# Kernel optimization log

Hardware: AMD Instinct MI355X
Metric: run time of the kernel (lower is better)

## Reference

```python
import jax, jax.numpy as jnp
import numpy as np

V, E, H = 50000, 200, 256
B, R, S, W = 16, 16, 16, 32


def gru_last(x, Wih, Whh, bih, bhh):
    """PyTorch-style GRU, return final hidden state.
    x: [N, T, D]; Wih: [3H, D]; Whh: [3H, H]. Gate order: r, z, n."""
    gx = jnp.einsum('ntd,gd->ntg', x, Wih) + bih  # precompute input gates [N,T,3H]
    h0 = jnp.zeros((x.shape[0], Whh.shape[1]), x.dtype)

    def step(h, gxt):
        gh = h @ Whh.T + bhh
        xr, xz, xn = jnp.split(gxt, 3, axis=-1)
        hr, hz, hn = jnp.split(gh, 3, axis=-1)
        r = jax.nn.sigmoid(xr + hr)
        z = jax.nn.sigmoid(xz + hz)
        n = jnp.tanh(xn + r * hn)
        return (1.0 - z) * n + z * h, None

    h, _ = jax.lax.scan(step, h0, jnp.swapaxes(gx, 0, 1))
    return h  # [N, H]


def mlp(x, W1, b1, W2, b2):
    # Linear -> SELU -> (Dropout is identity in eval) -> Linear
    return jax.nn.selu(x @ W1.T + b1) @ W2.T + b2


def setup_inputs() -> dict:
    key = jax.random.key(0)
    ks = jax.random.split(key, 20)
    n = lambda k, shp: (jax.random.normal(k, shp, dtype=jnp.float32) * 0.05)
    inp = {
        'inputs': jax.random.randint(ks[0], (B, R, S, W), 0, V, dtype=jnp.int64),
        'emb': n(ks[1], (V, E)),
        'w_Wih': n(ks[2], (3 * H, E)), 'w_Whh': n(ks[3], (3 * H, H)),
        'w_bih': n(ks[4], (3 * H,)), 'w_bhh': n(ks[5], (3 * H,)),
        's_Wih': n(ks[6], (3 * H, H)), 's_Whh': n(ks[7], (3 * H, H)),
        's_bih': n(ks[8], (3 * H,)), 's_bhh': n(ks[9], (3 * H,)),
        'r_Wih': n(ks[10], (3 * H, H)), 'r_Whh': n(ks[11], (3 * H, H)),
        'r_bih': n(ks[12], (3 * H,)), 'r_bhh': n(ks[13], (3 * H,)),
        'rfc_W1': n(ks[14], (H // 2, H)), 'rfc_b1': n(ks[15], (H // 2,)),
        'rfc_W2': n(ks[16], (1, H // 2)), 'rfc_b2': jnp.zeros((1,), jnp.float32),
        'pfc_W1': n(ks[17], (H // 2, H)), 'pfc_b1': n(ks[18], (H // 2,)),
        'pfc_W2': n(ks[19], (1, H // 2)), 'pfc_b2': jnp.zeros((1,), jnp.float32),
    }
    return inp


def reference(inputs, emb, w_Wih, w_Whh, w_bih, w_bhh,
              s_Wih, s_Whh, s_bih, s_bhh,
              r_Wih, r_Whh, r_bih, r_bhh,
              rfc_W1, rfc_b1, rfc_W2, rfc_b2,
              pfc_W1, pfc_b1, pfc_W2, pfc_b2):
    b, r, s, w = inputs.shape
    x = emb[inputs]                                   # [B,R,S,W,E] (dropout = identity in eval)
    # word-level GRU over all sentences at once (batches the Python double loop)
    sent_h = gru_last(x.reshape(b * r * s, w, E), w_Wih, w_Whh, w_bih, w_bhh)  # [B*R*S, H]
    # sentence-level GRU per review
    rev_h = gru_last(sent_h.reshape(b * r, s, H), s_Wih, s_Whh, s_bih, s_bhh)  # [B*R, H]
    p_batch = rev_h.reshape(b, r, H)                  # [B, R, H]
    r_stars = mlp(p_batch, rfc_W1, rfc_b1, rfc_W2, rfc_b2)  # [B, R, 1]
    # review-level GRU per business
    biz_h = gru_last(p_batch, r_Wih, r_Whh, r_bih, r_bhh)   # [B, H]
    b_stars = mlp(biz_h, pfc_W1, pfc_b1, pfc_W2, pfc_b2)    # [B, 1]
    return (b_stars, r_stars)
```

## Files before the change

### kernel.cpp

```cpp
#include <hip/hip_runtime.h>
#include <math.h>

#define VOCAB 50000
#define EDIM  200
#define HDIM  256
#define G3    768
#define NSEQ1 4096
#define T1    32
#define NSEQ2 256
#define T2    16
#define NSEQ3 16
#define T3    16

using bf16x8 = __attribute__((ext_vector_type(8))) short;
using f32x4  = __attribute__((ext_vector_type(4))) float;

__device__ __forceinline__ float sigmoid_f(float x) {
    return 1.0f / (1.0f + __expf(-x));
}
__device__ __forceinline__ float tanh_f(float x) {
    return 1.0f - 2.0f / (__expf(2.0f * x) + 1.0f);
}
__device__ __forceinline__ short f2b(float f) {
    unsigned u = __float_as_uint(f);
    unsigned r = (u + 0x7fffu + ((u >> 16) & 1u)) >> 16;
    return (short)r;
}

__global__ void convert_pad(const float* __restrict__ src, short* __restrict__ dst,
                            int Kin, int Kpad) {
    const int r = blockIdx.x;
    for (int k = threadIdx.x; k < Kpad; k += blockDim.x)
        dst[(size_t)r * Kpad + k] = (k < Kin) ? f2b(src[(size_t)r * Kin + k]) : (short)0;
}

template <int KC, bool AF32>
__global__ __launch_bounds__(512) void gemm_mfma(
    const void* __restrict__ Av, const short* __restrict__ WB,
    const float* __restrict__ bias, float* __restrict__ C,
    int M, int Keff) {
    constexpr int KPAD  = KC * 32;
    constexpr int CELLS = KPAD / 8;
    __shared__ short As[128 * 256];
    const int tid = threadIdx.x;
    const int m0 = blockIdx.x * 128;
    const int n0 = blockIdx.y * 192;

    {
        const int row  = tid >> 2;
        const int c0   = (tid & 3) * 8;
        const int rowg = m0 + row;
        const int vcell = Keff >> 3;
        for (int i = 0; i < 8; i++) {
            const int c = c0 + i;
            if (c >= CELLS) break;
            bf16x8 v;
            if (rowg < M && c < vcell) {
                if constexpr (AF32) {
                    const float* ap = (const float*)Av + (size_t)rowg * Keff + c * 8;
                    const float4 x = *(const float4*)ap;
                    const float4 y = *(const float4*)(ap + 4);
                    v[0] = f2b(x.x); v[1] = f2b(x.y); v[2] = f2b(x.z); v[3] = f2b(x.w);
                    v[4] = f2b(y.x); v[5] = f2b(y.y); v[6] = f2b(y.z); v[7] = f2b(y.w);
                } else {
                    const short* ap = (const short*)Av + (size_t)rowg * Keff + c * 8;
                    v = *(const bf16x8*)ap;
                }
            } else {
                v = (bf16x8)(short)0;
            }
            *(bf16x8*)&As[row * 256 + ((c ^ (row & 7)) << 3)] = v;
        }
    }
    __syncthreads();

    const int w  = tid >> 6;
    const int l  = tid & 63;
    const int lr = l & 15, lg = l >> 4;

    bf16x8 af[KC];
    {
        const int row = (w << 4) + lr;
#pragma unroll
        for (int kc = 0; kc < KC; kc++) {
            const int cell = kc * 4 + lg;
            af[kc] = *(const bf16x8*)&As[row * 256 + ((cell ^ (row & 7)) << 3)];
        }
    }
    f32x4 acc[12];
#pragma unroll
    for (int nt = 0; nt < 12; nt++) acc[nt] = (f32x4){0.f, 0.f, 0.f, 0.f};
#pragma unroll
    for (int nt = 0; nt < 12; nt++) {
        const short* wb = WB + (size_t)(n0 + nt * 16 + lr) * KPAD + lg * 8;
#pragma unroll
        for (int kc = 0; kc < KC; kc++) {
            bf16x8 bf = *(const bf16x8*)(wb + kc * 32);
            acc[nt] = __builtin_amdgcn_mfma_f32_16x16x32_bf16(af[kc], bf, acc[nt], 0, 0, 0);
        }
    }
#pragma unroll
    for (int nt = 0; nt < 12; nt++) {
        const int col = n0 + nt * 16 + lr;
        const float bv = bias[col];
#pragma unroll
        for (int q = 0; q < 4; q++) {
            const int row = m0 + (w << 4) + lg * 4 + q;
            if (row < M) C[(size_t)row * G3 + col] = acc[nt][q] + bv;
        }
    }
}

__global__ __launch_bounds__(512) void gru_mfma(
    const int* __restrict__ idx,
    const float* __restrict__ gxsrc,
    const short* __restrict__ WB,
    const float* __restrict__ bhh,
    float* __restrict__ hf32,
    short* __restrict__ hb16,
    int T) {
    __shared__ short hsB[16 * 256];
    const int tid = threadIdx.x;
    const int n0 = blockIdx.x * 16;
    const int w  = tid >> 6, l = tid & 63;
    const int lr = l & 15, lg = l >> 4;
    const int tt0 = w * 2;

    for (int i = tid; i < 16 * 256; i += 512) hsB[i] = 0;

    float bR[2], bZ[2], bN[2];
#pragma unroll
    for (int ti = 0; ti < 2; ti++) {
        const int jj = (tt0 + ti) * 16 + lr;
        bR[ti] = bhh[jj]; bZ[ti] = bhh[256 + jj]; bN[ti] = bhh[512 + jj];
    }
    float hreg[2][4] = {};
    int toks[4];
    if (idx) {
#pragma unroll
        for (int q = 0; q < 4; q++) toks[q] = idx[(size_t)(n0 + lg * 4 + q) * T];
    }
    __syncthreads();

    for (int t = 0; t < T; t++) {
        float gxv[2][4][3];
#pragma unroll
        for (int q = 0; q < 4; q++) {
            const size_t rowbase = idx ? (size_t)toks[q] * G3
                                       : ((size_t)(n0 + lg * 4 + q) * T + t) * G3;
#pragma unroll
            for (int ti = 0; ti < 2; ti++) {
                const int jj = (tt0 + ti) * 16 + lr;
                gxv[ti][q][0] = gxsrc[rowbase + jj];
                gxv[ti][q][1] = gxsrc[rowbase + 256 + jj];
                gxv[ti][q][2] = gxsrc[rowbase + 512 + jj];
            }
        }
        bf16x8 af[8];
#pragma unroll
        for (int kc = 0; kc < 8; kc++) {
            const int cell = kc * 4 + lg;
            af[kc] = *(const bf16x8*)&hsB[lr * 256 + ((cell ^ (lr & 7)) << 3)];
        }
        __syncthreads();

        f32x4 acc[2][3];
#pragma unroll
        for (int ti = 0; ti < 2; ti++)
#pragma unroll
            for (int g = 0; g < 3; g++) acc[ti][g] = (f32x4){0.f, 0.f, 0.f, 0.f};
#pragma unroll
        for (int ti = 0; ti < 2; ti++) {
#pragma unroll
            for (int g = 0; g < 3; g++) {
                const short* wb = WB + (size_t)(g * 256 + (tt0 + ti) * 16 + lr) * 256 + lg * 8;
#pragma unroll
                for (int kc = 0; kc < 8; kc++) {
                    bf16x8 bf = *(const bf16x8*)(wb + kc * 32);
                    acc[ti][g] = __builtin_amdgcn_mfma_f32_16x16x32_bf16(af[kc], bf, acc[ti][g], 0, 0, 0);
                }
            }
        }
        if (idx && t + 1 < T) {
#pragma unroll
            for (int q = 0; q < 4; q++) toks[q] = idx[(size_t)(n0 + lg * 4 + q) * T + t + 1];
        }
#pragma unroll
        for (int ti = 0; ti < 2; ti++) {
            const int jj = (tt0 + ti) * 16 + lr;
#pragma unroll
            for (int q = 0; q < 4; q++) {
                const float r = sigmoid_f(gxv[ti][q][0] + acc[ti][0][q] + bR[ti]);
                const float z = sigmoid_f(gxv[ti][q][1] + acc[ti][1][q] + bZ[ti]);
                const float n = tanh_f(gxv[ti][q][2] + r * (acc[ti][2][q] + bN[ti]));
                const float h = (1.f - z) * n + z * hreg[ti][q];
                hreg[ti][q] = h;
                const int s = lg * 4 + q;
                hsB[s * 256 + (((jj >> 3) ^ (s & 7)) << 3) + (jj & 7)] = f2b(h);
            }
        }
        __syncthreads();
    }
#pragma unroll
    for (int ti = 0; ti < 2; ti++) {
        const int jj = (tt0 + ti) * 16 + lr;
#pragma unroll
        for (int q = 0; q < 4; q++) {
            const int s = lg * 4 + q;
            const size_t o = (size_t)(n0 + s) * HDIM + jj;
            if (hf32) hf32[o] = hreg[ti][q];
            if (hb16) hb16[o] = f2b(hreg[ti][q]);
        }
    }
}

__global__ __launch_bounds__(128) void mlp_head(
    const float* __restrict__ hin, const float* __restrict__ W1,
    const float* __restrict__ b1, const float* __restrict__ W2,
    const float* __restrict__ b2, float* __restrict__ out) {
    const int row = blockIdx.x;
    const int gg = threadIdx.x;
    const float* h = hin + (size_t)row * HDIM;
    const float* wv1 = W1 + (size_t)gg * HDIM;
    float acc = 0.f;
#pragma unroll 4
    for (int k = 0; k < HDIM; k += 4) {
        const float4 hv = *(const float4*)&h[k];
        const float4 wv = *(const float4*)&wv1[k];
        acc += hv.x * wv.x; acc += hv.y * wv.y;
        acc += hv.z * wv.z; acc += hv.w * wv.w;
    }
    acc += b1[gg];
    const float alpha = 1.6732632423543772f;
    const float scale = 1.0507009873554805f;
    const float s = scale * (acc > 0.f ? acc : alpha * expm1f(acc));
    float v = s * W2[gg];

    __shared__ float red[128];
    red[gg] = v;
    __syncthreads();
    if (gg < 64) {
        float x = red[gg] + red[gg + 64];
#pragma unroll
        for (int off = 32; off; off >>= 1) x += __shfl_down(x, off);
        if (gg == 0) out[row] = x + b2[0];
    }
}

extern "C" void kernel_launch(void* const* d_in, const int* in_sizes, int n_in,
                              void* d_out, int out_size, void* d_ws, size_t ws_size,
                              hipStream_t stream) {
    const int*   idx    = (const int*)d_in[0];
    const float* emb    = (const float*)d_in[1];
    const float* w_Wih  = (const float*)d_in[2];
    const float* w_Whh  = (const float*)d_in[3];
    const float* w_bih  = (const float*)d_in[4];
    const float* w_bhh  = (const float*)d_in[5];
    const float* s_Wih  = (const float*)d_in[6];
    const float* s_Whh  = (const float*)d_in[7];
    const float* s_bih  = (const float*)d_in[8];
    const float* s_bhh  = (const float*)d_in[9];
    const float* r_Wih  = (const float*)d_in[10];
    const float* r_Whh  = (const float*)d_in[11];
    const float* r_bih  = (const float*)d_in[12];
    const float* r_bhh  = (const float*)d_in[13];
    const float* rfc_W1 = (const float*)d_in[14];
    const float* rfc_b1 = (const float*)d_in[15];
    const float* rfc_W2 = (const float*)d_in[16];
    const float* rfc_b2 = (const float*)d_in[17];
    const float* pfc_W1 = (const float*)d_in[18];
    const float* pfc_b1 = (const float*)d_in[19];
    const float* pfc_W2 = (const float*)d_in[20];
    const float* pfc_b2 = (const float*)d_in[21];

    float* out = (float*)d_out;

    float* fws = (float*)d_ws;
    float* P     = fws;
    float* gx2   = P     + (size_t)VOCAB * G3;
    float* rev_h = gx2   + (size_t)NSEQ1 * G3;
    float* gx3   = rev_h + (size_t)NSEQ2 * HDIM;
    float* biz_h = gx3   + (size_t)NSEQ2 * G3;
    short* sws = (short*)(biz_h + (size_t)NSEQ3 * HDIM);
    short* WhhB_w = sws;
    short* WihB_w = WhhB_w + (size_t)G3 * HDIM;
    short* sWihB  = WihB_w + (size_t)G3 * 224;
    short* sWhhB  = sWihB  + (size_t)G3 * HDIM;
    short* rWihB  = sWhhB  + (size_t)G3 * HDIM;
    short* rWhhB  = rWihB  + (size_t)G3 * HDIM;
    short* sent_hB = rWhhB + (size_t)G3 * HDIM;
    short* rev_hB  = sent_hB + (size_t)NSEQ1 * HDIM;

    convert_pad<<<G3, 256, 0, stream>>>(w_Whh, WhhB_w, HDIM, HDIM);
    convert_pad<<<G3, 256, 0, stream>>>(w_Wih, WihB_w, EDIM, 224);
    convert_pad<<<G3, 256, 0, stream>>>(s_Wih, sWihB, HDIM, HDIM);
    convert_pad<<<G3, 256, 0, stream>>>(s_Whh, sWhhB, HDIM, HDIM);
    convert_pad<<<G3, 256, 0, stream>>>(r_Wih, rWihB, HDIM, HDIM);
    convert_pad<<<G3, 256, 0, stream>>>(r_Whh, rWhhB, HDIM, HDIM);

    gemm_mfma<7, true><<<dim3((VOCAB + 127) / 128, 4), 512, 0, stream>>>(
        emb, WihB_w, w_bih, P, VOCAB, EDIM);

    gru_mfma<<<NSEQ1 / 16, 512, 0, stream>>>(
        idx, P, WhhB_w, w_bhh, nullptr, sent_hB, T1);

    gemm_mfma<8, false><<<dim3(NSEQ1 / 128, 4), 512, 0, stream>>>(
        sent_hB, sWihB, s_bih, gx2, NSEQ1, HDIM);

    gru_mfma<<<NSEQ2 / 16, 512, 0, stream>>>(
        nullptr, gx2, sWhhB, s_bhh, rev_h, rev_hB, T2);

    mlp_head<<<NSEQ2, 128, 0, stream>>>(
        rev_h, rfc_W1, rfc_b1, rfc_W2, rfc_b2, out + 16);

    gemm_mfma<8, false><<<dim3(2, 4), 512, 0, stream>>>(
        rev_hB, rWihB, r_bih, gx3, NSEQ2, HDIM);

    gru_mfma<<<1, 512, 0, stream>>>(
        nullptr, gx3, rWhhB, r_bhh, biz_h, nullptr, T3);

    mlp_head<<<NSEQ3, 128, 0, stream>>>(
        biz_h, pfc_W1, pfc_b1, pfc_W2, pfc_b2, out);
}
```

Baseline: 706.1 us.

## Store input-gate projections in bf16 and double-buffer them into LDS via async loads

```diff
diff --git a/kernel.cpp b/kernel.cpp
--- a/kernel.cpp
+++ b/kernel.cpp
@@ -26,6 +26,14 @@
     unsigned r = (u + 0x7fffu + ((u >> 16) & 1u)) >> 16;
     return (short)r;
 }
+__device__ __forceinline__ float b2f(unsigned short v) {
+    return __uint_as_float((unsigned)v << 16);
+}
+__device__ __forceinline__ void gload_lds16(const void* g, void* l) {
+    __builtin_amdgcn_global_load_lds(
+        (const __attribute__((address_space(1))) void*)g,
+        (__attribute__((address_space(3))) void*)l, 16, 0, 0);
+}
 
 __global__ void convert_pad(const float* __restrict__ src, short* __restrict__ dst,
                             int Kin, int Kpad) {
@@ -34,10 +42,10 @@
         dst[(size_t)r * Kpad + k] = (k < Kin) ? f2b(src[(size_t)r * Kin + k]) : (short)0;
 }
 
-template <int KC, bool AF32>
+template <int KC, bool AF32, bool CBF16>
 __global__ __launch_bounds__(512) void gemm_mfma(
     const void* __restrict__ Av, const short* __restrict__ WB,
-    const float* __restrict__ bias, float* __restrict__ C,
+    const float* __restrict__ bias, void* __restrict__ Cv,
     int M, int Keff) {
     constexpr int KPAD  = KC * 32;
     constexpr int CELLS = KPAD / 8;
@@ -106,20 +114,25 @@
 #pragma unroll
         for (int q = 0; q < 4; q++) {
             const int row = m0 + (w << 4) + lg * 4 + q;
-            if (row < M) C[(size_t)row * G3 + col] = acc[nt][q] + bv;
+            if (row < M) {
+                const float o = acc[nt][q] + bv;
+                if constexpr (CBF16) ((short*)Cv)[(size_t)row * G3 + col] = f2b(o);
+                else                 ((float*)Cv)[(size_t)row * G3 + col] = o;
+            }
         }
     }
 }
 
 __global__ __launch_bounds__(512) void gru_mfma(
     const int* __restrict__ idx,
-    const float* __restrict__ gxsrc,
+    const short* __restrict__ gxb,
     const short* __restrict__ WB,
     const float* __restrict__ bhh,
     float* __restrict__ hf32,
     short* __restrict__ hb16,
     int T) {
     __shared__ short hsB[16 * 256];
+    __shared__ short gxs[2][16 * 768];
     const int tid = threadIdx.x;
     const int n0 = blockIdx.x * 16;
     const int w  = tid >> 6, l = tid & 63;
@@ -135,34 +148,47 @@
         bR[ti] = bhh[jj]; bZ[ti] = bhh[256 + jj]; bN[ti] = bhh[512 + jj];
     }
     float hreg[2][4] = {};
-    int toks[4];
-    if (idx) {
-#pragma unroll
-        for (int q = 0; q < 4; q++) toks[q] = idx[(size_t)(n0 + lg * 4 + q) * T];
-    }
+
+    auto stage = [&](short* dstbase, int t) {
+#pragma unroll
+        for (int it = 0; it < 3; it++) {
+            const int g = it * 8192 + (tid << 4);
+            const int s = g / 1536;
+            const int cb = g - s * 1536;
+            size_t rowbase;
+            if (idx) {
+                int tk = idx[(size_t)(n0 + s) * T + t];
+                tk = min(max(tk, 0), VOCAB - 1);
+                rowbase = (size_t)tk * 1536;
+            } else {
+                rowbase = ((size_t)(n0 + s) * T + t) * 1536;
+            }
+            const int cell = cb >> 4;
+            const int sb = ((cell ^ (s & 7)) << 4) | (cb & 15);
+            const char* src = (const char*)gxb + rowbase + sb;
+            char* dst = (char*)dstbase + it * 8192 + (w << 10);
+            gload_lds16(src, dst);
+        }
+    };
+    auto gx_at = [&](const short* buf, int s, int col) -> float {
+        const int cb = col << 1;
+        const int addr = s * 1536 + ((((cb >> 4) ^ (s & 7)) << 4) | (cb & 15));
+        return b2f(*(const unsigned short*)((const char*)buf + addr));
+    };
+
+    stage(gxs[0], 0);
     __syncthreads();
 
+    int cur = 0;
     for (int t = 0; t < T; t++) {
-        float gxv[2][4][3];
-#pragma unroll
-        for (int q = 0; q < 4; q++) {
-            const size_t rowbase = idx ? (size_t)toks[q] * G3
-                                       : ((size_t)(n0 + lg * 4 + q) * T + t) * G3;
-#pragma unroll
-            for (int ti = 0; ti < 2; ti++) {
-                const int jj = (tt0 + ti) * 16 + lr;
-                gxv[ti][q][0] = gxsrc[rowbase + jj];
-                gxv[ti][q][1] = gxsrc[rowbase + 256 + jj];
-                gxv[ti][q][2] = gxsrc[rowbase + 512 + jj];
-            }
-        }
+        if (t + 1 < T) stage(gxs[cur ^ 1], t + 1);
+
         bf16x8 af[8];
 #pragma unroll
         for (int kc = 0; kc < 8; kc++) {
             const int cell = kc * 4 + lg;
             af[kc] = *(const bf16x8*)&hsB[lr * 256 + ((cell ^ (lr & 7)) << 3)];
         }
-        __syncthreads();
 
         f32x4 acc[2][3];
 #pragma unroll
@@ -181,26 +207,29 @@
                 }
             }
         }
-        if (idx && t + 1 < T) {
-#pragma unroll
-            for (int q = 0; q < 4; q++) toks[q] = idx[(size_t)(n0 + lg * 4 + q) * T + t + 1];
-        }
+        __syncthreads();
+
 #pragma unroll
         for (int ti = 0; ti < 2; ti++) {
             const int jj = (tt0 + ti) * 16 + lr;
 #pragma unroll
             for (int q = 0; q < 4; q++) {
-                const float r = sigmoid_f(gxv[ti][q][0] + acc[ti][0][q] + bR[ti]);
-                const float z = sigmoid_f(gxv[ti][q][1] + acc[ti][1][q] + bZ[ti]);
-                const float n = tanh_f(gxv[ti][q][2] + r * (acc[ti][2][q] + bN[ti]));
+                const int s = lg * 4 + q;
+                const float xr = gx_at(gxs[cur], s, jj);
+                const float xz = gx_at(gxs[cur], s, 256 + jj);
+                const float xn = gx_at(gxs[cur], s, 512 + jj);
+                const float r = sigmoid_f(xr + acc[ti][0][q] + bR[ti]);
+                const float z = sigmoid_f(xz + acc[ti][1][q] + bZ[ti]);
+                const float n = tanh_f(xn + r * (acc[ti][2][q] + bN[ti]));
                 const float h = (1.f - z) * n + z * hreg[ti][q];
                 hreg[ti][q] = h;
-                const int s = lg * 4 + q;
                 hsB[s * 256 + (((jj >> 3) ^ (s & 7)) << 3) + (jj & 7)] = f2b(h);
             }
         }
         __syncthreads();
-    }
+        cur ^= 1;
+    }
+
 #pragma unroll
     for (int ti = 0; ti < 2; ti++) {
         const int jj = (tt0 + ti) * 16 + lr;
@@ -275,21 +304,21 @@
 
     float* out = (float*)d_out;
 
-    float* fws = (float*)d_ws;
-    float* P     = fws;
-    float* gx2   = P     + (size_t)VOCAB * G3;
-    float* rev_h = gx2   + (size_t)NSEQ1 * G3;
-    float* gx3   = rev_h + (size_t)NSEQ2 * HDIM;
-    float* biz_h = gx3   + (size_t)NSEQ2 * G3;
-    short* sws = (short*)(biz_h + (size_t)NSEQ3 * HDIM);
-    short* WhhB_w = sws;
-    short* WihB_w = WhhB_w + (size_t)G3 * HDIM;
-    short* sWihB  = WihB_w + (size_t)G3 * 224;
-    short* sWhhB  = sWihB  + (size_t)G3 * HDIM;
-    short* rWihB  = sWhhB  + (size_t)G3 * HDIM;
-    short* rWhhB  = rWihB  + (size_t)G3 * HDIM;
-    short* sent_hB = rWhhB + (size_t)G3 * HDIM;
+    short* sws = (short*)d_ws;
+    short* Pb      = sws;
+    short* gx2b    = Pb      + (size_t)VOCAB * G3;
+    short* gx3b    = gx2b    + (size_t)NSEQ1 * G3;
+    short* WhhB_w  = gx3b    + (size_t)NSEQ2 * G3;
+    short* WihB_w  = WhhB_w  + (size_t)G3 * HDIM;
+    short* sWihB   = WihB_w  + (size_t)G3 * 224;
+    short* sWhhB   = sWihB   + (size_t)G3 * HDIM;
+    short* rWihB   = sWhhB   + (size_t)G3 * HDIM;
+    short* rWhhB   = rWihB   + (size_t)G3 * HDIM;
+    short* sent_hB = rWhhB   + (size_t)G3 * HDIM;
     short* rev_hB  = sent_hB + (size_t)NSEQ1 * HDIM;
+    float* fws     = (float*)(rev_hB + (size_t)NSEQ2 * HDIM);
+    float* rev_h   = fws;
+    float* biz_h   = rev_h + (size_t)NSEQ2 * HDIM;
 
     convert_pad<<<G3, 256, 0, stream>>>(w_Whh, WhhB_w, HDIM, HDIM);
     convert_pad<<<G3, 256, 0, stream>>>(w_Wih, WihB_w, EDIM, 224);
@@ -298,26 +327,26 @@
     convert_pad<<<G3, 256, 0, stream>>>(r_Wih, rWihB, HDIM, HDIM);
     convert_pad<<<G3, 256, 0, stream>>>(r_Whh, rWhhB, HDIM, HDIM);
 
-    gemm_mfma<7, true><<<dim3((VOCAB + 127) / 128, 4), 512, 0, stream>>>(
-        emb, WihB_w, w_bih, P, VOCAB, EDIM);
+    gemm_mfma<7, true, true><<<dim3((VOCAB + 127) / 128, 4), 512, 0, stream>>>(
+        emb, WihB_w, w_bih, Pb, VOCAB, EDIM);
 
     gru_mfma<<<NSEQ1 / 16, 512, 0, stream>>>(
-        idx, P, WhhB_w, w_bhh, nullptr, sent_hB, T1);
-
-    gemm_mfma<8, false><<<dim3(NSEQ1 / 128, 4), 512, 0, stream>>>(
-        sent_hB, sWihB, s_bih, gx2, NSEQ1, HDIM);
+        idx, Pb, WhhB_w, w_bhh, nullptr, sent_hB, T1);
+
+    gemm_mfma<8, false, true><<<dim3(NSEQ1 / 128, 4), 512, 0, stream>>>(
+        sent_hB, sWihB, s_bih, gx2b, NSEQ1, HDIM);
 
     gru_mfma<<<NSEQ2 / 16, 512, 0, stream>>>(
-        nullptr, gx2, sWhhB, s_bhh, rev_h, rev_hB, T2);
+        nullptr, gx2b, sWhhB, s_bhh, rev_h, rev_hB, T2);
 
     mlp_head<<<NSEQ2, 128, 0, stream>>>(
         rev_h, rfc_W1, rfc_b1, rfc_W2, rfc_b2, out + 16);
 
-    gemm_mfma<8, false><<<dim3(2, 4), 512, 0, stream>>>(
-        rev_hB, rWihB, r_bih, gx3, NSEQ2, HDIM);
+    gemm_mfma<8, false, true><<<dim3(2, 4), 512, 0, stream>>>(
+        rev_hB, rWihB, r_bih, gx3b, NSEQ2, HDIM);
 
     gru_mfma<<<1, 512, 0, stream>>>(
-        nullptr, gx3, rWhhB, r_bhh, biz_h, nullptr, T3);
+        nullptr, gx3b, rWhhB, r_bhh, biz_h, nullptr, T3);
 
     mlp_head<<<NSEQ3, 128, 0, stream>>>(
         biz_h, pfc_W1, pfc_b1, pfc_W2, pfc_b2, out);
```

Result: slower. 975.4 us (+38.1%).
